# Optimization experiments

Measured on AMD Instinct MI355X. Metric: run time of the kernel, lower is better.

The kernel has to match this reference:

```python
import jax, jax.numpy as jnp
import numpy as np

MARGIN = 1.0


def setup_inputs() -> dict:
    key = jax.random.key(0)
    k1, k2 = jax.random.split(key)
    inputs = jax.random.normal(k1, (512, 256), dtype=jnp.float32)
    targets = jax.random.randint(k2, (512,), 0, 64)
    return {"inputs": inputs, "targets": targets}


def reference(inputs, targets):
    n = inputs.shape[0]
    # pairwise euclidean distance matrix [n, n]
    sq = jnp.sum(inputs * inputs, axis=1)
    dist = sq[:, None] + sq[None, :] - 2.0 * (inputs @ inputs.T)
    dist = jnp.sqrt(jnp.clip(dist, 1e-16))

    # triplet margins: ap_dist[i,j] - an_dist[i,k] + margin -> [n, n, n]
    triplet = dist[:, :, None] - dist[:, None, :] + MARGIN

    # mask: i != j, i != k, j != k, labels[i]==labels[j], labels[i]!=labels[k]
    not_eye = ~jnp.eye(n, dtype=bool)
    dist_idx = not_eye[:, :, None] & not_eye[:, None, :] & not_eye[None, :, :]
    teq = targets[:, None] == targets[None, :]  # symmetric [n, n]
    valid = teq[:, :, None] & (~teq[:, None, :])
    mask = (valid & dist_idx).astype(triplet.dtype)

    triplet = jnp.maximum(mask * triplet, 0.0)
    num_triplets = jnp.sum((triplet > 1e-16).astype(triplet.dtype))
    return jnp.sum(triplet) / (num_triplets + 1e-16)
```

## Files before the change

kernel.cpp:

```cpp
#include <hip/hip_runtime.h>

constexpr int N = 512;
constexpr int D = 256;
#define MARGIN 1.0f

#define ACC(S, A, B)                                                   \
  { float ex = A.x - B.x, ey = A.y - B.y, ez = A.z - B.z,              \
          ew = A.w - B.w;                                              \
    S += ex * ex + ey * ey + ez * ez + ew * ew; }

__global__ __launch_bounds__(1024, 4) void triplet_fused(
    const float* __restrict__ x, const int* __restrict__ tgt,
    float* __restrict__ part) {
  __shared__ __align__(16) float m0[N], m1[N];
  __shared__ float cl0[N], cl1[N];
  __shared__ int nv0, nv1;
  __shared__ float wred[32];

  const int b = blockIdx.x;
  const int i0 = 2 * b, i1 = 2 * b + 1;
  const int tid = threadIdx.x;
  const int wave = tid >> 6, lane = tid & 63;
  const int sub = lane & 15, rg = lane >> 4;
  const int t0 = tgt[i0], t1 = tgt[i1];

  if (tid == 0) { nv0 = 0; nv1 = 0; }

  const float4* xa = (const float4*)(x + (size_t)i0 * D);
  const float4* xc = (const float4*)(x + (size_t)i1 * D);
  float4 a0 = xa[sub], a1 = xa[16 + sub], a2 = xa[32 + sub], a3 = xa[48 + sub];
  float4 c0 = xc[sub], c1 = xc[16 + sub], c2 = xc[32 + sub], c3 = xc[48 + sub];
  __syncthreads();

  const int rot = (b * 171) & (N - 1);
  const int rbase = wave * 32 + rg;
  #pragma unroll 2
  for (int it = 0; it < 8; ++it) {
    const int r = (rbase + it * 4 + rot) & (N - 1);
    const float4* xr = (const float4*)(x + (size_t)r * D);
    float4 b0 = xr[sub];
    float4 b1 = xr[16 + sub];
    float4 b2 = xr[32 + sub];
    float4 b3 = xr[48 + sub];
    float sa = 0.f, sb = 0.f;
    ACC(sa, a0, b0); ACC(sa, a1, b1); ACC(sa, a2, b2); ACC(sa, a3, b3);
    ACC(sb, c0, b0); ACC(sb, c1, b1); ACC(sb, c2, b2); ACC(sb, c3, b3);
    #pragma unroll
    for (int off = 8; off > 0; off >>= 1) {
      sa += __shfl_down(sa, off);
      sb += __shfl_down(sb, off);
    }
    if (sub == 0) {
      const int tj = tgt[r];
      float da = sqrtf(fmaxf(sa, 1e-16f));
      float db = sqrtf(fmaxf(sb, 1e-16f));
      m0[r] = (tj != t0) ? da : __builtin_inff();
      m1[r] = (tj != t1) ? db : __builtin_inff();
      if (tj == t0 && r != i0) { int s = atomicAdd(&nv0, 1); cl0[s] = da + MARGIN; }
      if (tj == t1 && r != i1) { int s = atomicAdd(&nv1, 1); cl1[s] = db + MARGIN; }
    }
  }
  __syncthreads();

  float sum = 0.f, cnt = 0.f;
  const int e = tid & 511, half = tid >> 9;
  const float mk0 = m0[e], mk1 = m1[e];
  const int n0 = nv0, n1 = nv1;
  for (int v = half; v < n0; v += 2) {
    float a = cl0[v] - mk0;
    sum += fmaxf(a, 0.f);
    cnt += (a > 1e-16f ? 1.f : 0.f);
  }
  for (int v = half; v < n1; v += 2) {
    float a = cl1[v] - mk1;
    sum += fmaxf(a, 0.f);
    cnt += (a > 1e-16f ? 1.f : 0.f);
  }

  #pragma unroll
  for (int off = 32; off > 0; off >>= 1) {
    sum += __shfl_down(sum, off);
    cnt += __shfl_down(cnt, off);
  }
  if (lane == 0) { wred[wave] = sum; wred[16 + wave] = cnt; }
  __syncthreads();
  if (tid == 0) {
    float s = 0.f, c = 0.f;
    #pragma unroll
    for (int w = 0; w < 16; ++w) { s += wred[w]; c += wred[16 + w]; }
    part[2 * b] = s;
    part[2 * b + 1] = c;
  }
}

__global__ __launch_bounds__(256) void triplet_finalize(
    const float* __restrict__ part, float* __restrict__ out) {
  __shared__ float wred[8];
  const int tid = threadIdx.x;
  float s = part[2 * tid], c = part[2 * tid + 1];
  #pragma unroll
  for (int off = 32; off > 0; off >>= 1) {
    s += __shfl_down(s, off);
    c += __shfl_down(c, off);
  }
  int wave = tid >> 6, lane = tid & 63;
  if (lane == 0) { wred[wave] = s; wred[4 + wave] = c; }
  __syncthreads();
  if (tid == 0) {
    float ts = wred[0] + wred[1] + wred[2] + wred[3];
    float tc = wred[4] + wred[5] + wred[6] + wred[7];
    out[0] = ts / (tc + 1e-16f);
  }
}

extern "C" void kernel_launch(void* const* d_in, const int* in_sizes, int n_in,
                              void* d_out, int out_size, void* d_ws, size_t ws_size,
                              hipStream_t stream) {
  const float* x = (const float*)d_in[0];
  const int* tgt = (const int*)d_in[1];
  float* out = (float*)d_out;
  float* part = (float*)d_ws;

  triplet_fused<<<N / 2, 1024, 0, stream>>>(x, tgt, part);
  triplet_finalize<<<1, 256, 0, stream>>>(part, out);
}
```

Before: 66.00 us.

## Split into tiled distance kernel and triplet kernel with last-block reduction

Distance computation moves to its own kernel. Each block holds 8 anchor rows in registers and computes a 8x128 distance tile using the norm expansion, so each streamed row is reused across 8 anchors instead of 2. The triplet kernel reads the precomputed distance matrix and now runs 512 threads per block. The separate finalize launch is replaced by a ticket-based last-block reduction. The cost is a global round-trip for the 1 MB distance matrix and heavy register use from 32 float4 values per thread.

```diff
diff --git a/kernel.cpp b/kernel.cpp
--- a/kernel.cpp
+++ b/kernel.cpp
@@ -4,75 +4,112 @@
 constexpr int D = 256;
 #define MARGIN 1.0f
 
-#define ACC(S, A, B)                                                   \
-  { float ex = A.x - B.x, ey = A.y - B.y, ez = A.z - B.z,              \
-          ew = A.w - B.w;                                              \
-    S += ex * ex + ey * ey + ez * ez + ew * ew; }
+__device__ __forceinline__ float dot4(const float4 a, const float4 b) {
+  return a.x * b.x + a.y * b.y + a.z * b.z + a.w * b.w;
+}
 
-__global__ __launch_bounds__(1024, 4) void triplet_fused(
-    const float* __restrict__ x, const int* __restrict__ tgt,
-    float* __restrict__ part) {
-  __shared__ __align__(16) float m0[N], m1[N];
+__global__ __launch_bounds__(512, 2) void dist_kernel(
+    const float* __restrict__ x, float* __restrict__ dist,
+    int* __restrict__ ticket) {
+  const int b = blockIdx.x;
+  const int at = b >> 2;
+  const int ct = b & 3;
+  const int tid = threadIdx.x;
+  const int wave = tid >> 6, lane = tid & 63;
+  const int sub = lane & 15, rg = lane >> 4;
+
+  if (b == 0 && tid == 0) *ticket = 0;
+
+  float4 fa[8][4];
+  #pragma unroll
+  for (int a = 0; a < 8; ++a) {
+    const float4* xa = (const float4*)(x + (size_t)(8 * at + a) * D);
+    #pragma unroll
+    for (int q = 0; q < 4; ++q) fa[a][q] = xa[q * 16 + sub];
+  }
+  float sqa[8];
+  #pragma unroll
+  for (int a = 0; a < 8; ++a) {
+    float s = dot4(fa[a][0], fa[a][0]) + dot4(fa[a][1], fa[a][1]) +
+              dot4(fa[a][2], fa[a][2]) + dot4(fa[a][3], fa[a][3]);
+    #pragma unroll
+    for (int m = 1; m < 16; m <<= 1) s += __shfl_xor(s, m);
+    sqa[a] = s;
+  }
+
+  __shared__ float dtile[8][132];
+
+  #pragma unroll 2
+  for (int it = 0; it < 4; ++it) {
+    const int l = wave * 16 + it * 4 + rg;
+    const float4* xr = (const float4*)(x + (size_t)(ct * 128 + l) * D);
+    float4 b0 = xr[sub], b1 = xr[16 + sub], b2 = xr[32 + sub],
+           b3 = xr[48 + sub];
+    float nr = dot4(b0, b0) + dot4(b1, b1) + dot4(b2, b2) + dot4(b3, b3);
+    float dp[8];
+    #pragma unroll
+    for (int a = 0; a < 8; ++a)
+      dp[a] = dot4(fa[a][0], b0) + dot4(fa[a][1], b1) + dot4(fa[a][2], b2) +
+              dot4(fa[a][3], b3);
+    #pragma unroll
+    for (int m = 1; m < 16; m <<= 1) {
+      nr += __shfl_xor(nr, m);
+      #pragma unroll
+      for (int a = 0; a < 8; ++a) dp[a] += __shfl_xor(dp[a], m);
+    }
+    if (sub < 8) {
+      float ds = dp[0], qs = sqa[0];
+      #pragma unroll
+      for (int a = 1; a < 8; ++a)
+        if (sub == a) { ds = dp[a]; qs = sqa[a]; }
+      const float dd = qs + nr - 2.0f * ds;
+      dtile[sub][l] = sqrtf(fmaxf(dd, 1e-16f));
+    }
+  }
+  __syncthreads();
+  for (int j = tid; j < 8 * 128; j += 512) {
+    const int a = j >> 7, l = j & 127;
+    dist[(size_t)(8 * at + a) * N + ct * 128 + l] = dtile[a][l];
+  }
+}
+
+__global__ __launch_bounds__(512, 2) void triplet_kernel(
+    const float* __restrict__ dist, const int* __restrict__ tgt,
+    float* __restrict__ psum, float* __restrict__ pcnt,
+    int* __restrict__ ticket, float* __restrict__ out) {
   __shared__ float cl0[N], cl1[N];
   __shared__ int nv0, nv1;
-  __shared__ float wred[32];
+  __shared__ float wred[16];
+  __shared__ int lastf;
 
   const int b = blockIdx.x;
   const int i0 = 2 * b, i1 = 2 * b + 1;
   const int tid = threadIdx.x;
   const int wave = tid >> 6, lane = tid & 63;
-  const int sub = lane & 15, rg = lane >> 4;
-  const int t0 = tgt[i0], t1 = tgt[i1];
+  const int e = tid;
 
   if (tid == 0) { nv0 = 0; nv1 = 0; }
-
-  const float4* xa = (const float4*)(x + (size_t)i0 * D);
-  const float4* xc = (const float4*)(x + (size_t)i1 * D);
-  float4 a0 = xa[sub], a1 = xa[16 + sub], a2 = xa[32 + sub], a3 = xa[48 + sub];
-  float4 c0 = xc[sub], c1 = xc[16 + sub], c2 = xc[32 + sub], c3 = xc[48 + sub];
+  const int t0 = tgt[i0], t1 = tgt[i1];
+  const int tj = tgt[e];
+  const float d0 = dist[(size_t)i0 * N + e];
+  const float d1 = dist[(size_t)i1 * N + e];
   __syncthreads();
 
-  const int rot = (b * 171) & (N - 1);
-  const int rbase = wave * 32 + rg;
-  #pragma unroll 2
-  for (int it = 0; it < 8; ++it) {
-    const int r = (rbase + it * 4 + rot) & (N - 1);
-    const float4* xr = (const float4*)(x + (size_t)r * D);
-    float4 b0 = xr[sub];
-    float4 b1 = xr[16 + sub];
-    float4 b2 = xr[32 + sub];
-    float4 b3 = xr[48 + sub];
-    float sa = 0.f, sb = 0.f;
-    ACC(sa, a0, b0); ACC(sa, a1, b1); ACC(sa, a2, b2); ACC(sa, a3, b3);
-    ACC(sb, c0, b0); ACC(sb, c1, b1); ACC(sb, c2, b2); ACC(sb, c3, b3);
-    #pragma unroll
-    for (int off = 8; off > 0; off >>= 1) {
-      sa += __shfl_down(sa, off);
-      sb += __shfl_down(sb, off);
-    }
-    if (sub == 0) {
-      const int tj = tgt[r];
-      float da = sqrtf(fmaxf(sa, 1e-16f));
-      float db = sqrtf(fmaxf(sb, 1e-16f));
-      m0[r] = (tj != t0) ? da : __builtin_inff();
-      m1[r] = (tj != t1) ? db : __builtin_inff();
-      if (tj == t0 && r != i0) { int s = atomicAdd(&nv0, 1); cl0[s] = da + MARGIN; }
-      if (tj == t1 && r != i1) { int s = atomicAdd(&nv1, 1); cl1[s] = db + MARGIN; }
-    }
-  }
+  const float m0 = (tj != t0) ? d0 : __builtin_inff();
+  const float m1 = (tj != t1) ? d1 : __builtin_inff();
+  if (tj == t0 && e != i0) { int s = atomicAdd(&nv0, 1); cl0[s] = d0 + MARGIN; }
+  if (tj == t1 && e != i1) { int s = atomicAdd(&nv1, 1); cl1[s] = d1 + MARGIN; }
   __syncthreads();
 
   float sum = 0.f, cnt = 0.f;
-  const int e = tid & 511, half = tid >> 9;
-  const float mk0 = m0[e], mk1 = m1[e];
   const int n0 = nv0, n1 = nv1;
-  for (int v = half; v < n0; v += 2) {
-    float a = cl0[v] - mk0;
+  for (int v = 0; v < n0; ++v) {
+    const float a = cl0[v] - m0;
     sum += fmaxf(a, 0.f);
     cnt += (a > 1e-16f ? 1.f : 0.f);
   }
-  for (int v = half; v < n1; v += 2) {
-    float a = cl1[v] - mk1;
+  for (int v = 0; v < n1; ++v) {
+    const float a = cl1[v] - m1;
     sum += fmaxf(a, 0.f);
     cnt += (a > 1e-16f ? 1.f : 0.f);
   }
@@ -82,34 +119,37 @@
     sum += __shfl_down(sum, off);
     cnt += __shfl_down(cnt, off);
   }
-  if (lane == 0) { wred[wave] = sum; wred[16 + wave] = cnt; }
+  if (lane == 0) { wred[wave] = sum; wred[8 + wave] = cnt; }
   __syncthreads();
   if (tid == 0) {
     float s = 0.f, c = 0.f;
     #pragma unroll
-    for (int w = 0; w < 16; ++w) { s += wred[w]; c += wred[16 + w]; }
-    part[2 * b] = s;
-    part[2 * b + 1] = c;
+    for (int w = 0; w < 8; ++w) { s += wred[w]; c += wred[8 + w]; }
+    psum[b] = s;
+    pcnt[b] = c;
+    __threadfence();
+    const int old = atomicAdd(ticket, 1);
+    lastf = (old == 255) ? 1 : 0;
   }
-}
+  __syncthreads();
 
-__global__ __launch_bounds__(256) void triplet_finalize(
-    const float* __restrict__ part, float* __restrict__ out) {
-  __shared__ float wred[8];
-  const int tid = threadIdx.x;
-  float s = part[2 * tid], c = part[2 * tid + 1];
-  #pragma unroll
-  for (int off = 32; off > 0; off >>= 1) {
-    s += __shfl_down(s, off);
-    c += __shfl_down(c, off);
-  }
-  int wave = tid >> 6, lane = tid & 63;
-  if (lane == 0) { wred[wave] = s; wred[4 + wave] = c; }
-  __syncthreads();
-  if (tid == 0) {
-    float ts = wred[0] + wred[1] + wred[2] + wred[3];
-    float tc = wred[4] + wred[5] + wred[6] + wred[7];
-    out[0] = ts / (tc + 1e-16f);
+  if (lastf) {
+    __threadfence();
+    float s = (tid < 256) ? psum[tid] : 0.f;
+    float c = (tid < 256) ? pcnt[tid] : 0.f;
+    #pragma unroll
+    for (int off = 32; off > 0; off >>= 1) {
+      s += __shfl_down(s, off);
+      c += __shfl_down(c, off);
+    }
+    if (lane == 0) { wred[wave] = s; wred[8 + wave] = c; }
+    __syncthreads();
+    if (tid == 0) {
+      float ts = 0.f, tc = 0.f;
+      #pragma unroll
+      for (int w = 0; w < 8; ++w) { ts += wred[w]; tc += wred[8 + w]; }
+      out[0] = ts / (tc + 1e-16f);
+    }
   }
 }
 
@@ -119,8 +159,13 @@
   const float* x = (const float*)d_in[0];
   const int* tgt = (const int*)d_in[1];
   float* out = (float*)d_out;
-  float* part = (float*)d_ws;
 
-  triplet_fused<<<N / 2, 1024, 0, stream>>>(x, tgt, part);
-  triplet_finalize<<<1, 256, 0, stream>>>(part, out);
+  float* wsf = (float*)d_ws;
+  float* psum = wsf;
+  float* pcnt = wsf + 256;
+  int* ticket = (int*)(wsf + 512);
+  float* dist = wsf + 1024;
+
+  dist_kernel<<<256, 512, 0, stream>>>(x, dist, ticket);
+  triplet_kernel<<<256, 512, 0, stream>>>(dist, tgt, psum, pcnt, ticket, out);
 }
```

New measurement: 73.17 us. 1.11x slower.

## Prefetch next row, reduce with DPP row shifts, stage targets in LDS

Applied to the files above, without the earlier changes.

Software-pipelines the distance loop so the next row's float4 loads are issued before the current row is reduced, hiding global load latency. The 16-lane shuffle reduction is replaced with DPP row_shr adds, with the total read from lane 15. Targets are copied into shared memory once per block instead of being read from global memory inside the loop. This costs extra registers for the prefetch buffers and performs one redundant wrap-around load on the last iteration.

```diff
diff --git a/kernel.cpp b/kernel.cpp
--- a/kernel.cpp
+++ b/kernel.cpp
@@ -3,6 +3,18 @@
 constexpr int N = 512;
 constexpr int D = 256;
 #define MARGIN 1.0f
+
+__device__ __forceinline__ float dpp_add16(float v) {
+  v += __int_as_float(__builtin_amdgcn_update_dpp(
+      0, __float_as_int(v), 0x118, 0xF, 0xF, true));
+  v += __int_as_float(__builtin_amdgcn_update_dpp(
+      0, __float_as_int(v), 0x114, 0xF, 0xF, true));
+  v += __int_as_float(__builtin_amdgcn_update_dpp(
+      0, __float_as_int(v), 0x112, 0xF, 0xF, true));
+  v += __int_as_float(__builtin_amdgcn_update_dpp(
+      0, __float_as_int(v), 0x111, 0xF, 0xF, true));
+  return v;
+}
 
 #define ACC(S, A, B)                                                   \
   { float ex = A.x - B.x, ey = A.y - B.y, ez = A.z - B.z,              \
@@ -14,6 +26,7 @@
     float* __restrict__ part) {
   __shared__ __align__(16) float m0[N], m1[N];
   __shared__ float cl0[N], cl1[N];
+  __shared__ int ts[N];
   __shared__ int nv0, nv1;
   __shared__ float wred[32];
 
@@ -22,36 +35,37 @@
   const int tid = threadIdx.x;
   const int wave = tid >> 6, lane = tid & 63;
   const int sub = lane & 15, rg = lane >> 4;
-  const int t0 = tgt[i0], t1 = tgt[i1];
 
   if (tid == 0) { nv0 = 0; nv1 = 0; }
+  if (tid < N) ts[tid] = tgt[tid];
 
   const float4* xa = (const float4*)(x + (size_t)i0 * D);
   const float4* xc = (const float4*)(x + (size_t)i1 * D);
   float4 a0 = xa[sub], a1 = xa[16 + sub], a2 = xa[32 + sub], a3 = xa[48 + sub];
   float4 c0 = xc[sub], c1 = xc[16 + sub], c2 = xc[32 + sub], c3 = xc[48 + sub];
   __syncthreads();
+  const int t0 = ts[i0], t1 = ts[i1];
 
   const int rot = (b * 171) & (N - 1);
   const int rbase = wave * 32 + rg;
+
+  int r = (rbase + rot) & (N - 1);
+  const float4* xr = (const float4*)(x + (size_t)r * D);
+  float4 b0 = xr[sub], b1 = xr[16 + sub], b2 = xr[32 + sub], b3 = xr[48 + sub];
+
   #pragma unroll 2
   for (int it = 0; it < 8; ++it) {
-    const int r = (rbase + it * 4 + rot) & (N - 1);
-    const float4* xr = (const float4*)(x + (size_t)r * D);
-    float4 b0 = xr[sub];
-    float4 b1 = xr[16 + sub];
-    float4 b2 = xr[32 + sub];
-    float4 b3 = xr[48 + sub];
+    const int rn = (rbase + (((it + 1) & 7) << 2) + rot) & (N - 1);
+    const float4* xn = (const float4*)(x + (size_t)rn * D);
+    float4 p0 = xn[sub], p1 = xn[16 + sub], p2 = xn[32 + sub], p3 = xn[48 + sub];
+
     float sa = 0.f, sb = 0.f;
     ACC(sa, a0, b0); ACC(sa, a1, b1); ACC(sa, a2, b2); ACC(sa, a3, b3);
     ACC(sb, c0, b0); ACC(sb, c1, b1); ACC(sb, c2, b2); ACC(sb, c3, b3);
-    #pragma unroll
-    for (int off = 8; off > 0; off >>= 1) {
-      sa += __shfl_down(sa, off);
-      sb += __shfl_down(sb, off);
-    }
-    if (sub == 0) {
-      const int tj = tgt[r];
+    sa = dpp_add16(sa);
+    sb = dpp_add16(sb);
+    if (sub == 15) {
+      const int tj = ts[r];
       float da = sqrtf(fmaxf(sa, 1e-16f));
       float db = sqrtf(fmaxf(sb, 1e-16f));
       m0[r] = (tj != t0) ? da : __builtin_inff();
@@ -59,6 +73,8 @@
       if (tj == t0 && r != i0) { int s = atomicAdd(&nv0, 1); cl0[s] = da + MARGIN; }
       if (tj == t1 && r != i1) { int s = atomicAdd(&nv1, 1); cl1[s] = db + MARGIN; }
     }
+    b0 = p0; b1 = p1; b2 = p2; b3 = p3;
+    r = rn;
   }
   __syncthreads();
 
```

Result: no change. 64.87 us (-1.7%).
